# Kernel tuning notes

Measured on AMD Instinct MI355X. Metric: run time of the kernel, lower is better.

Reference implementation:

```python
import jax, jax.numpy as jnp
import numpy as np
from jax import lax

B, N, C = 8, 16384, 4
NUM_GROUPS = 128
GROUP_SIZE = 32
GROUP_RADIUS = 0.1
UPSCALE_K = 128
OVERLAP_FACTOR = 0.7


def setup_inputs() -> dict:
    key = jax.random.key(0)
    k1, k2 = jax.random.split(key)
    # xyz in [0,1]^3, energy in [0,1] at channel 3
    points = jax.random.uniform(k1, (B, N, C), dtype=jnp.float32)
    lengths = jax.random.randint(k2, (B,), N // 2, N + 1).astype(jnp.int32)
    return {"points": points, "lengths": lengths}


def _fps(xyz, lengths, K):
    """Farthest point sampling. xyz: (B,N,3) -> centers (B,K,3), idx (B,K)."""
    B_, N_, _ = xyz.shape
    valid = jnp.arange(N_)[None, :] < lengths[:, None]          # (B,N)
    mind0 = jnp.where(valid, jnp.inf, -jnp.inf)                 # running min dist
    start = jnp.zeros((B_,), jnp.int32)                         # fixed start point
    batch = jnp.arange(B_)

    def step(carry, _):
        mind, cur = carry
        c = xyz[batch, cur]                                     # (B,3)
        d = jnp.sum((xyz - c[:, None, :]) ** 2, axis=-1)        # (B,N)
        mind = jnp.minimum(mind, jnp.where(valid, d, -jnp.inf))
        nxt = jnp.argmax(mind, axis=1).astype(jnp.int32)
        return (mind, nxt), cur

    _, idxs = lax.scan(step, (mind0, start), None, length=K)
    idxs = idxs.T                                               # (B,K)
    centers = xyz[batch[:, None], idxs]                         # (B,K,3)
    return centers, idxs


def _cnms(centers, radius, overlap_factor):
    """Greedy cluster-NMS over FPS-ordered centers. Returns keep mask (B,G)."""
    B_, G, _ = centers.shape
    d2 = jnp.sum((centers[:, :, None, :] - centers[:, None, :, :]) ** 2, axis=-1)
    thr = (2.0 * radius * (1.0 - overlap_factor)) ** 2          # spheres overlap > factor

    def step(keep, j):
        conflict = jnp.any(keep & (d2[:, j, :] < thr), axis=-1)
        keep = keep.at[:, j].set(~conflict)
        return keep, None

    keep, _ = lax.scan(step, jnp.zeros((B_, G), bool), jnp.arange(G))
    return keep


def _ball_query(centers, xyz, lengths, retain, K, radius):
    """First-K points within radius of each center (pytorch3d semantics); -1 pad."""
    N_ = xyz.shape[1]
    d2 = jnp.sum((centers[:, :, None, :] - xyz[:, None, :, :]) ** 2, axis=-1)  # (B,G,N)
    in_len = (jnp.arange(N_)[None, :] < lengths[:, None])[:, None, :]
    valid = (d2 <= radius * radius) & in_len & retain[:, :, None]
    # pick the K smallest point indices among valid ones -> "first K found"
    key_ = jnp.where(valid, jnp.arange(N_, dtype=jnp.int32)[None, None, :], N_)
    negv, _ = lax.top_k(-key_, K)                               # (B,G,K)
    idx = -negv
    return jnp.where(idx == N_, -1, idx)


def reference(points, lengths):
    xyz = points[..., :3]
    centers, _ = _fps(xyz, lengths, NUM_GROUPS)                 # (B,G,3)
    retain = _cnms(centers, GROUP_RADIUS, OVERLAP_FACTOR)       # (B,G)
    idx = _ball_query(centers, xyz, lengths, retain, UPSCALE_K, GROUP_RADIUS)

    # select_topk_by_energy (energies_idx = 3)
    batch = jnp.arange(points.shape[0])[:, None, None]
    invalid = idx == -1
    energies = jnp.where(invalid, -jnp.inf, points[batch, jnp.clip(idx, 0), 3])
    topv, topi = lax.top_k(energies, GROUP_SIZE)                # (B,G,K_new)
    tidx = jnp.take_along_axis(idx, topi, axis=2)
    tidx = jnp.where(jnp.isneginf(topv), -1, tidx)

    # fill_empty_indices: replace -1 with the group's first index
    fidx = jnp.where(tidx == -1, tidx[:, :, :1], tidx)

    # masked_gather: -1 -> gather 0 then zero out
    groups = points[batch, jnp.clip(fidx, 0)]                   # (B,G,K,C)
    groups = jnp.where((fidx == -1)[..., None], 0.0, groups)

    group_lengths = jnp.sum(jnp.all(tidx != -1, axis=2), axis=1)  # (B,)
    embedding_mask = jnp.arange(NUM_GROUPS)[None, :] < group_lengths[:, None]

    # center xyz channels, then scale ALL channels by radius (as in source)
    groups = groups.at[..., :3].add(-centers[:, :, None, :])
    groups = groups / GROUP_RADIUS
    return groups, centers, embedding_mask
```

## Files before the change

### kernel.cpp

```cpp
#include <hip/hip_runtime.h>
#include <math.h>

#define B_ 8
#define N_ 16384
#define G_ 128
#define GS_ 32
#define UK_ 128
#define FPS_T 1024
#define FPS_W 16
#define PPT 16
#define BQ_T 512
#define BQ_W 8

#pragma clang fp contract(off)

typedef float v2f __attribute__((ext_vector_type(2)));

#define DPP64_MAXSTEP(vv, ctrl, rmask)                                          \
  {                                                                             \
    unsigned _lo = (unsigned)__builtin_amdgcn_update_dpp(                       \
        0, (int)(unsigned)((vv) & 0xffffffffull), (ctrl), (rmask), 0xf, false); \
    unsigned _hi = (unsigned)__builtin_amdgcn_update_dpp(                       \
        0, (int)(unsigned)((vv) >> 32), (ctrl), (rmask), 0xf, false);           \
    unsigned long long _tv = ((unsigned long long)_hi << 32) | _lo;             \
    if (_tv > (vv)) (vv) = _tv;                                                 \
  }

__device__ __forceinline__ float dist2(float x, float y, float z,
                                       float cx, float cy, float cz) {
    float dx = __fsub_rn(x, cx);
    float dy = __fsub_rn(y, cy);
    float dz = __fsub_rn(z, cz);
    return __fadd_rn(__fadd_rn(__fmul_rn(dx, dx), __fmul_rn(dy, dy)),
                     __fmul_rn(dz, dz));
}

__global__ void init_kernel(int* __restrict__ gl) {
    int t = threadIdx.x;
    if (t < B_) gl[t] = 0;
}

__global__ __launch_bounds__(FPS_T, 4) void fps_cnms_kernel(
    const float4* __restrict__ pts, const int* __restrict__ lengths,
    float* __restrict__ centers_out, int* __restrict__ keep_out) {
    const int b = blockIdx.x;
    const int t = threadIdx.x;
    const int lane = t & 63;
    const int wv = t >> 6;
    const int len = lengths[b];
    const float4* p = pts + (size_t)b * N_;

    __shared__ float4 s_xy4[N_ / 2];
    __shared__ __align__(16) unsigned long long s_part[2][FPS_W];
    __shared__ float s_cen[G_][3];

    v2f zp[PPT / 2];
    v2f mp[PPT / 2];
#pragma unroll
    for (int j = 0; j < PPT / 2; j++) {
        int nA = (2 * j) * FPS_T + t;
        int nB = nA + FPS_T;
        float4 qA = p[nA];
        float4 qB = p[nB];
        s_xy4[j * FPS_T + t] = make_float4(qA.x, qB.x, qA.y, qB.y);
        v2f zz; zz.x = qA.z; zz.y = qB.z;
        zp[j] = zz;
        v2f mm;
        mm.x = (nA < len) ? INFINITY : -INFINITY;
        mm.y = (nB < len) ? INFINITY : -INFINITY;
        mp[j] = mm;
    }
#pragma unroll
    for (int j = 0; j < PPT / 2; j++) asm volatile("" : "+v"(zp[j]));
    __syncthreads();

    int n = 0;
    for (int k = 0; k < G_; k++) {
        float4 c = p[n];
        if (t == 0) {
            centers_out[(b * G_ + k) * 3 + 0] = c.x;
            centers_out[(b * G_ + k) * 3 + 1] = c.y;
            centers_out[(b * G_ + k) * 3 + 2] = c.z;
            s_cen[k][0] = c.x; s_cen[k][1] = c.y; s_cen[k][2] = c.z;
        }
        if (k == G_ - 1) break;

        v2f cXX, cYY, cZZ;
        cXX.x = c.x; cXX.y = c.x;
        cYY.x = c.y; cYY.y = c.y;
        cZZ.x = c.z; cZZ.y = c.z;

#pragma unroll
        for (int j = 0; j < PPT / 2; j++) {
            float4 xy = s_xy4[j * FPS_T + t];
            v2f xv, yv;
            xv.x = xy.x; xv.y = xy.y;
            yv.x = xy.z; yv.y = xy.w;
            v2f dx = xv - cXX;
            v2f dy = yv - cYY;
            v2f dz = zp[j] - cZZ;
            v2f dd = (dx * dx + dy * dy) + dz * dz;
            mp[j].x = fminf(mp[j].x, dd.x);
            mp[j].y = fminf(mp[j].y, dd.y);
        }

        float bv = mp[0].x;
#pragma unroll
        for (int j = 0; j < PPT / 2; j++) {
            if (j > 0) bv = fmaxf(bv, mp[j].x);
            bv = fmaxf(bv, mp[j].y);
        }
        int bi = 0;
#pragma unroll
        for (int s = PPT - 1; s >= 0; s--) {
            float mv = (s & 1) ? mp[s >> 1].y : mp[s >> 1].x;
            if (mv == bv) bi = s;
        }

        unsigned u = __float_as_uint(bv);
        u = (u & 0x80000000u) ? ~u : (u | 0x80000000u);
        int bn = (bi << 10) | t;
        unsigned long long v = ((unsigned long long)u << 32) | (unsigned)(~bn);

        DPP64_MAXSTEP(v, 0x111, 0xf);
        DPP64_MAXSTEP(v, 0x112, 0xf);
        DPP64_MAXSTEP(v, 0x114, 0xf);
        DPP64_MAXSTEP(v, 0x118, 0xf);
        DPP64_MAXSTEP(v, 0x142, 0xa);
        DPP64_MAXSTEP(v, 0x143, 0xc);
        if (lane == 63) s_part[k & 1][wv] = v;
        __syncthreads();

        unsigned long long m = s_part[k & 1][lane & 15];
        DPP64_MAXSTEP(m, 0x111, 0xf);
        DPP64_MAXSTEP(m, 0x112, 0xf);
        DPP64_MAXSTEP(m, 0x114, 0xf);
        DPP64_MAXSTEP(m, 0x118, 0xf);
        unsigned wlo = (unsigned)__builtin_amdgcn_readlane(
            (int)(unsigned)(m & 0xffffffffull), 15);
        n = (int)(~wlo);
    }

    __syncthreads();

    if (t < 64) {
        const float THR = (float)((2.0 * 0.1 * (1.0 - 0.7)) * (2.0 * 0.1 * (1.0 - 0.7)));
        float ax = s_cen[t][0],      ay = s_cen[t][1],      az = s_cen[t][2];
        float ex = s_cen[t + 64][0], ey = s_cen[t + 64][1], ez = s_cen[t + 64][2];
        bool k0 = false, k1 = false;
        for (int j = 0; j < G_; j++) {
            float jx = s_cen[j][0], jy = s_cen[j][1], jz = s_cen[j][2];
            bool c0 = k0 && (dist2(ax, ay, az, jx, jy, jz) < THR);
            bool c1 = k1 && (dist2(ex, ey, ez, jx, jy, jz) < THR);
            bool conflict = __any(c0 || c1);
            if (j == t)      k0 = !conflict;
            if (j == t + 64) k1 = !conflict;
        }
        keep_out[b * G_ + t]      = k0 ? 1 : 0;
        keep_out[b * G_ + t + 64] = k1 ? 1 : 0;
    }
}

__global__ __launch_bounds__(BQ_T) void group_kernel(
    const float4* __restrict__ pts, const int* __restrict__ lengths,
    const float* __restrict__ centers, const int* __restrict__ keep,
    float* __restrict__ groups_out, int* __restrict__ gl) {
    const int bid = blockIdx.x;
    const int b = bid >> 7;
    const int t = threadIdx.x;
    const int lane = t & 63;
    const int wv = t >> 6;

    const float cx = centers[bid * 3 + 0];
    const float cy = centers[bid * 3 + 1];
    const float cz = centers[bid * 3 + 2];
    float4* out4 = (float4*)(groups_out + (size_t)bid * GS_ * 4);

    if (!keep[bid]) {
        if (t < GS_) {
            float4 o;
            o.x = __fdiv_rn(__fsub_rn(0.f, cx), 0.1f);
            o.y = __fdiv_rn(__fsub_rn(0.f, cy), 0.1f);
            o.z = __fdiv_rn(__fsub_rn(0.f, cz), 0.1f);
            o.w = 0.f;
            out4[t] = o;
        }
        return;
    }

    __shared__ int   s_widx[BQ_W][UK_];
    __shared__ float s_wen[BQ_W][UK_];
    __shared__ int   s_wcnt[BQ_W];
    __shared__ int   s_list[UK_];
    __shared__ float s_en[UK_];
    __shared__ int   s_ord[GS_];

    const int len = lengths[b];
    const float R2 = (float)(0.1 * 0.1);
    const float4* p = pts + (size_t)b * N_;

    {
        const int base0 = wv * (N_ / BQ_W);
        int cnt = 0;
        for (int it = 0; it < (N_ / BQ_W) / 64; it++) {
            int n = base0 + it * 64 + lane;
            float4 q = p[n];
            float d2 = dist2(q.x, q.y, q.z, cx, cy, cz);
            bool pred = (n < len) && (d2 <= R2);
            unsigned long long m = __ballot(pred);
            int prefix = __popcll(m & ((1ull << lane) - 1ull));
            int slot = cnt + prefix;
            if (pred && slot < UK_) { s_widx[wv][slot] = n; s_wen[wv][slot] = q.w; }
            cnt += __popcll(m);
        }
        if (lane == 0) s_wcnt[wv] = (cnt < UK_) ? cnt : UK_;
    }
    __syncthreads();

    int M = 0;
#pragma unroll
    for (int w = 0; w < BQ_W; w++) M += s_wcnt[w];
    if (M > UK_) M = UK_;

    if (t < UK_ && t < M) {
        int j = t, w = 0;
        while (w < BQ_W - 1 && j >= s_wcnt[w]) { j -= s_wcnt[w]; w++; }
        s_list[t] = s_widx[w][j];
        s_en[t]   = s_wen[w][j];
    }
    __syncthreads();

    if (wv == 0) {
        float v0 = (lane < M) ? s_en[lane] : -INFINITY;
        float v1 = (lane + 64 < M) ? s_en[lane + 64] : -INFINITY;
        for (int k = 0; k < GS_; k++) {
            float bv; int bs;
            if (v0 >= v1) { bv = v0; bs = lane; }
            else          { bv = v1; bs = lane + 64; }
#pragma unroll
            for (int off = 32; off; off >>= 1) {
                float ov = __shfl_xor(bv, off);
                int   os = __shfl_xor(bs, off);
                bool tk = (ov > bv) || (ov == bv && os < bs);
                bv = tk ? ov : bv; bs = tk ? os : bs;
            }
            if (lane == 0) s_ord[k] = (bv == -INFINITY) ? -1 : bs;
            if (bs == lane)           v0 = -INFINITY;
            else if (bs == lane + 64) v1 = -INFINITY;
        }
    }
    __syncthreads();

    if (t < GS_) {
        int o0 = s_ord[0];
        int first = (o0 >= 0) ? s_list[o0] : -1;
        int ok = s_ord[t];
        int ti = (ok >= 0) ? s_list[ok] : -1;
        int f = (ti == -1) ? first : ti;
        float px = 0.f, py = 0.f, pz = 0.f, pw = 0.f;
        if (f >= 0) { float4 q = p[f]; px = q.x; py = q.y; pz = q.z; pw = q.w; }
        float4 o;
        o.x = __fdiv_rn(__fsub_rn(px, cx), 0.1f);
        o.y = __fdiv_rn(__fsub_rn(py, cy), 0.1f);
        o.z = __fdiv_rn(__fsub_rn(pz, cz), 0.1f);
        o.w = __fdiv_rn(pw, 0.1f);
        out4[t] = o;
    }
    if (t == 0 && M >= GS_) atomicAdd(&gl[b], 1);
}

__global__ void mask_kernel(const int* __restrict__ gl, float* __restrict__ mask_out) {
    int t = threadIdx.x;
    int b = t >> 7, g = t & 127;
    mask_out[t] = (g < gl[b]) ? 1.0f : 0.0f;
}

extern "C" void kernel_launch(void* const* d_in, const int* in_sizes, int n_in,
                              void* d_out, int out_size, void* d_ws, size_t ws_size,
                              hipStream_t stream) {
    const float4* pts = (const float4*)d_in[0];
    const int* lengths = (const int*)d_in[1];
    float* out = (float*)d_out;
    float* groups = out;
    float* centers = out + (size_t)B_ * G_ * GS_ * 4;
    float* mask = centers + (size_t)B_ * G_ * 3;
    int* keep = (int*)d_ws;
    int* gl = keep + B_ * G_;

    hipLaunchKernelGGL(init_kernel, dim3(1), dim3(64), 0, stream, gl);
    hipLaunchKernelGGL(fps_cnms_kernel, dim3(B_), dim3(FPS_T), 0, stream,
                       pts, lengths, centers, keep);
    hipLaunchKernelGGL(group_kernel, dim3(B_ * G_), dim3(BQ_T), 0, stream,
                       pts, lengths, centers, keep, groups, gl);
    hipLaunchKernelGGL(mask_kernel, dim3(1), dim3(B_ * G_), 0, stream, gl, mask);
}
```

Before: 318.6 us.

## Halve FPS block to 512 threads with 32 points each and tree max

Halves the FPS block to 512 threads (8 waves), each holding 32 points in registers instead of 16. The cross-wave reduction shrinks from 16 to 8 partials, dropping one DPP step, and the per-thread max becomes a balanced tree of packed v2f elementwise max/min ops rather than a serial chain. The aim is to cut barrier and reduction cost per FPS iteration, at the cost of more serial per-thread work and higher register pressure.

```diff
diff --git a/kernel.cpp b/kernel.cpp
--- a/kernel.cpp
+++ b/kernel.cpp
@@ -6,9 +6,9 @@
 #define G_ 128
 #define GS_ 32
 #define UK_ 128
-#define FPS_T 1024
-#define FPS_W 16
-#define PPT 16
+#define FPS_T 512
+#define FPS_W 8
+#define PPT 32
 #define BQ_T 512
 #define BQ_W 8
 
@@ -40,7 +40,7 @@
     if (t < B_) gl[t] = 0;
 }
 
-__global__ __launch_bounds__(FPS_T, 4) void fps_cnms_kernel(
+__global__ __launch_bounds__(FPS_T, 2) void fps_cnms_kernel(
     const float4* __restrict__ pts, const int* __restrict__ lengths,
     float* __restrict__ centers_out, int* __restrict__ keep_out) {
     const int b = blockIdx.x;
@@ -85,31 +85,35 @@
         }
         if (k == G_ - 1) break;
 
-        v2f cXX, cYY, cZZ;
-        cXX.x = c.x; cXX.y = c.x;
-        cYY.x = c.y; cYY.y = c.y;
-        cZZ.x = c.z; cZZ.y = c.z;
+        v2f cXX = {c.x, c.x};
+        v2f cYY = {c.y, c.y};
+        v2f cZZ = {c.z, c.z};
 
 #pragma unroll
         for (int j = 0; j < PPT / 2; j++) {
             float4 xy = s_xy4[j * FPS_T + t];
-            v2f xv, yv;
-            xv.x = xy.x; xv.y = xy.y;
-            yv.x = xy.z; yv.y = xy.w;
+            v2f xv = {xy.x, xy.y};
+            v2f yv = {xy.z, xy.w};
             v2f dx = xv - cXX;
             v2f dy = yv - cYY;
             v2f dz = zp[j] - cZZ;
             v2f dd = (dx * dx + dy * dy) + dz * dz;
-            mp[j].x = fminf(mp[j].x, dd.x);
-            mp[j].y = fminf(mp[j].y, dd.y);
-        }
-
-        float bv = mp[0].x;
-#pragma unroll
-        for (int j = 0; j < PPT / 2; j++) {
-            if (j > 0) bv = fmaxf(bv, mp[j].x);
-            bv = fmaxf(bv, mp[j].y);
-        }
+            mp[j] = __builtin_elementwise_min(mp[j], dd);
+        }
+
+        v2f t8[8];
+#pragma unroll
+        for (int j = 0; j < 8; j++)
+            t8[j] = __builtin_elementwise_max(mp[2 * j], mp[2 * j + 1]);
+        v2f t4a = __builtin_elementwise_max(t8[0], t8[1]);
+        v2f t4b = __builtin_elementwise_max(t8[2], t8[3]);
+        v2f t4c = __builtin_elementwise_max(t8[4], t8[5]);
+        v2f t4d = __builtin_elementwise_max(t8[6], t8[7]);
+        v2f t2a = __builtin_elementwise_max(t4a, t4b);
+        v2f t2b = __builtin_elementwise_max(t4c, t4d);
+        v2f t1 = __builtin_elementwise_max(t2a, t2b);
+        float bv = fmaxf(t1.x, t1.y);
+
         int bi = 0;
 #pragma unroll
         for (int s = PPT - 1; s >= 0; s--) {
@@ -119,7 +123,7 @@
 
         unsigned u = __float_as_uint(bv);
         u = (u & 0x80000000u) ? ~u : (u | 0x80000000u);
-        int bn = (bi << 10) | t;
+        int bn = (bi << 9) | t;
         unsigned long long v = ((unsigned long long)u << 32) | (unsigned)(~bn);
 
         DPP64_MAXSTEP(v, 0x111, 0xf);
@@ -131,13 +135,12 @@
         if (lane == 63) s_part[k & 1][wv] = v;
         __syncthreads();
 
-        unsigned long long m = s_part[k & 1][lane & 15];
+        unsigned long long m = s_part[k & 1][lane & 7];
         DPP64_MAXSTEP(m, 0x111, 0xf);
         DPP64_MAXSTEP(m, 0x112, 0xf);
         DPP64_MAXSTEP(m, 0x114, 0xf);
-        DPP64_MAXSTEP(m, 0x118, 0xf);
         unsigned wlo = (unsigned)__builtin_amdgcn_readlane(
-            (int)(unsigned)(m & 0xffffffffull), 15);
+            (int)(unsigned)(m & 0xffffffffull), 7);
         n = (int)(~wlo);
     }
 
```

New measurement: 311.0 us. -2.4%, faster.
